# Kernel optimization log

Hardware: AMD Instinct MI355X
Metric: run time of the kernel (lower is better)

The kernel has to match this reference:

```python
import jax, jax.numpy as jnp
import numpy as np

B, N, LQ, DK, DV, DD = 2, 16, 512, 64, 64, 128
TEMPERATURE = 8.0  # sqrt(DK)
NEG_INF = -1e9


def setup_inputs() -> dict:
    key = jax.random.key(0)
    ks = jax.random.split(key, 9)
    h2 = 2 * DD  # dc hidden width = d0 + d1
    return {
        "q": jax.random.normal(ks[0], (B, N, LQ, DK), jnp.float32),
        "k": jax.random.normal(ks[1], (B, N, LQ, DK), jnp.float32),
        "v": jax.random.normal(ks[2], (B, N, LQ, DV), jnp.float32),
        "d0": jax.random.normal(ks[3], (B, LQ, DD), jnp.float32),
        "d1": jax.random.normal(ks[4], (B, LQ, DD), jnp.float32),
        "W1": jax.random.normal(ks[5], (h2, h2), jnp.float32) / np.sqrt(h2),
        "b1": jnp.zeros((h2,), jnp.float32),
        "W2": jax.random.normal(ks[6], (h2, 2), jnp.float32) / np.sqrt(h2),
        "b2": jnp.zeros((2,), jnp.float32),
    }


def reference(q, k, v, d0, d1, W1, b1, W2, b2):
    b, n, lq, dk = q.shape
    dd = d0.shape[-1]
    # pairwise features: f[b,i,j] = concat(d0[b,i], d1[b,j])  -> [b,lq,lq,2dd]
    f = jnp.concatenate(
        [
            jnp.broadcast_to(d0[:, :, None, :], (b, lq, lq, dd)),
            jnp.broadcast_to(d1[:, None, :, :], (b, lq, lq, dd)),
        ],
        axis=-1,
    )
    h = jax.nn.relu(jnp.einsum("bijf,fg->bijg", f, W1) + b1)
    logits = jnp.einsum("bijg,gc->bijc", h, W2) + b2  # [b,lq,lq,2]
    # eval-mode gumbel_softmax(hard=True, tau=1, training=False): argmax of logits
    decisions = (jnp.argmax(logits, axis=-1) == 1)[:, None, :, :]  # [b,1,lq,lq]
    attn = jnp.einsum("bnid,bnjd->bnij", q / TEMPERATURE, k)
    attn = jnp.where(decisions, attn, NEG_INF)
    attn = jax.nn.softmax(attn, axis=-1)  # dropout is identity in eval mode
    output = jnp.einsum("bnij,bnjd->bnid", attn, v)
    return output, attn, decisions
```

## Files before the change

kernel.cpp:

```cpp
#include <hip/hip_runtime.h>

#define BB 2
#define NN 16
#define LQ 512
#define DKk 64
#define DVv 64
#define DDd 128
#define H2 256
#define NEG_INF -1e9f

__global__ __launch_bounds__(256) void mlp_stage1(
    const float* __restrict__ d0, const float* __restrict__ d1,
    const float* __restrict__ W1, const float* __restrict__ b1,
    double* __restrict__ U64, double* __restrict__ W64,
    float* __restrict__ U32, float* __restrict__ W32)
{
    __shared__ float drow[2][DDd];
    int gid = blockIdx.x;
    int half = gid >> 9;
    int r0 = (gid & 511) * 2;
    const float* din = half ? d1 : d0;
    int w1off = half ? DDd : 0;
    double* o64 = half ? W64 : U64;
    float* o32 = half ? W32 : U32;
    int t = threadIdx.x;
    drow[t >> 7][t & 127] = din[(size_t)(r0 + (t >> 7)) * DDd + (t & 127)];
    __syncthreads();
    int g = t;
    double acc[2] = {};
#pragma unroll 2
    for (int f = 0; f < DDd; f += 4) {
        double w0 = (double)W1[(w1off + f + 0) * H2 + g];
        double w1 = (double)W1[(w1off + f + 1) * H2 + g];
        double w2 = (double)W1[(w1off + f + 2) * H2 + g];
        double w3 = (double)W1[(w1off + f + 3) * H2 + g];
#pragma unroll
        for (int r = 0; r < 2; ++r) {
            float4 dr = *(const float4*)&drow[r][f];
            acc[r] = fma((double)dr.x, w0, acc[r]);
            acc[r] = fma((double)dr.y, w1, acc[r]);
            acc[r] = fma((double)dr.z, w2, acc[r]);
            acc[r] = fma((double)dr.w, w3, acc[r]);
        }
    }
    double bb = half ? 0.0 : (double)b1[g];
#pragma unroll
    for (int r = 0; r < 2; ++r) {
        double a = acc[r] + bb;
        o64[(size_t)(r0 + r) * H2 + g] = a;
        o32[(size_t)(r0 + r) * H2 + g] = (float)a;
    }
}

__global__ __launch_bounds__(256, 2) void dec_full(
    const float* __restrict__ U32, const float* __restrict__ W32,
    const double* __restrict__ U64, const double* __restrict__ W64,
    const float* __restrict__ W2, const float* __restrict__ b2,
    float* __restrict__ dec_out)
{
    __shared__ __align__(16) float Ut[H2][36];
    __shared__ __align__(16) float Wt[H2][36];
    __shared__ float gvs[H2];
    __shared__ int lbuf[1024];
    __shared__ int lcnt;
    int bid = blockIdx.x;
    int b  = bid >> 8;
    int i0 = ((bid >> 4) & 15) * 32;
    int j0 = (bid & 15) * 32;
    int t = threadIdx.x;
    gvs[t] = W2[t * 2 + 1] - W2[t * 2];
    if (t == 0) lcnt = 0;
    float bias = b2[1] - b2[0];
    {
        int r = t >> 3, gq = t & 7;
        const float* su = U32 + ((size_t)(b * LQ) + i0 + r) * H2;
        const float* sw = W32 + ((size_t)(b * LQ) + j0 + r) * H2;
#pragma unroll
        for (int s = 0; s < 8; ++s) {
            int g = gq * 4 + s * 32;
            float4 u4 = *(const float4*)(su + g);
            Ut[g + 0][r] = u4.x; Ut[g + 1][r] = u4.y;
            Ut[g + 2][r] = u4.z; Ut[g + 3][r] = u4.w;
            float4 w4 = *(const float4*)(sw + g);
            Wt[g + 0][r] = w4.x; Wt[g + 1][r] = w4.y;
            Wt[g + 2][r] = w4.z; Wt[g + 3][r] = w4.w;
        }
    }
    __syncthreads();
    int pi = t >> 4, pj = t & 15;
    float a00 = 0.f, a01 = 0.f, a10 = 0.f, a11 = 0.f;
#pragma unroll 8
    for (int g = 0; g < H2; ++g) {
        float2 u2 = *(const float2*)&Ut[g][pi * 2];
        float2 w2 = *(const float2*)&Wt[g][pj * 2];
        float gv = gvs[g];
        a00 = fmaf(fmaxf(u2.x + w2.x, 0.f), gv, a00);
        a01 = fmaf(fmaxf(u2.x + w2.y, 0.f), gv, a01);
        a10 = fmaf(fmaxf(u2.y + w2.x, 0.f), gv, a10);
        a11 = fmaf(fmaxf(u2.y + w2.y, 0.f), gv, a11);
    }
    int row0 = b * LQ + i0 + pi * 2;
    float g00 = a00 + bias, g01 = a01 + bias;
    float g10 = a10 + bias, g11 = a11 + bias;
    int jb = j0 + pj * 2;
    *(float2*)&dec_out[(size_t)row0 * LQ + jb] =
        make_float2(g00 > 0.f ? 1.f : 0.f, g01 > 0.f ? 1.f : 0.f);
    *(float2*)&dec_out[(size_t)(row0 + 1) * LQ + jb] =
        make_float2(g10 > 0.f ? 1.f : 0.f, g11 > 0.f ? 1.f : 0.f);
    if (fabsf(g00) < 2e-2f) { int lx = atomicAdd(&lcnt, 1); lbuf[lx] = (row0 << 9) | jb; }
    if (fabsf(g01) < 2e-2f) { int lx = atomicAdd(&lcnt, 1); lbuf[lx] = (row0 << 9) | (jb + 1); }
    if (fabsf(g10) < 2e-2f) { int lx = atomicAdd(&lcnt, 1); lbuf[lx] = ((row0 + 1) << 9) | jb; }
    if (fabsf(g11) < 2e-2f) { int lx = atomicAdd(&lcnt, 1); lbuf[lx] = ((row0 + 1) << 9) | (jb + 1); }
    __syncthreads();
    int nloc = lcnt;
    int wv = t >> 6, ln = t & 63;
    for (int x = wv; x < nloc; x += 4) {
        int pij = lbuf[x];
        int j = pij & (LQ - 1);
        int prow = pij >> 9;
        int pb = prow >> 9;
        const double* u = U64 + (size_t)prow * H2;
        const double* w = W64 + ((size_t)(pb * LQ) + j) * H2;
        double acc = 0.0;
        for (int g = ln; g < H2; g += 64) {
            double tv = u[g] + w[g];
            tv = tv > 0.0 ? tv : 0.0;
            acc = fma(tv, (double)W2[g * 2 + 1] - (double)W2[g * 2 + 0], acc);
        }
#pragma unroll
        for (int off = 32; off; off >>= 1) acc += __shfl_xor(acc, off, 64);
        if (ln == 0) {
            acc += (double)b2[1] - (double)b2[0];
            dec_out[(size_t)prow * LQ + j] = acc > 0.0 ? 1.f : 0.f;
        }
    }
}

__global__ __launch_bounds__(256) void fused_attn(
    const float* __restrict__ q, const float* __restrict__ k,
    const float* __restrict__ v, const float* __restrict__ dec,
    float* __restrict__ attn, float* __restrict__ out)
{
    __shared__ __align__(16) float smem[10752];
    float* qT = smem;
    float* kT = smem + 2304;
    float* Ps = smem;
    float* Vs = smem + 2112;
    int bid = blockIdx.x;
    int bn = bid >> 4;
    int i0 = (bid & 15) * 32;
    int b = bn >> 4;
    int t = threadIdx.x;

    {
        int qi = t >> 3;
        const float* src = q + ((size_t)bn * LQ + i0 + qi) * DKk;
#pragma unroll
        for (int it = 0; it < 2; ++it) {
            int kkq = (t & 7) + it * 8;
            float4 t4 = *(const float4*)(src + kkq * 4);
            qT[(kkq * 4 + 0) * 36 + qi] = t4.x;
            qT[(kkq * 4 + 1) * 36 + qi] = t4.y;
            qT[(kkq * 4 + 2) * 36 + qi] = t4.z;
            qT[(kkq * 4 + 3) * 36 + qi] = t4.w;
        }
    }
    int tiq = t >> 5;
    int tjq = t & 31;
    float s[4][4][4];

#pragma unroll
    for (int c = 0; c < 4; ++c) {
        __syncthreads();
        {
            int kj = t >> 2;
#pragma unroll
            for (int it = 0; it < 8; ++it) {
                int jj = kj + (it & 1) * 64;
                int kkq = (t & 3) + (it >> 1) * 4;
                float4 t4 = *(const float4*)(k + ((size_t)bn * LQ + c * 128 + jj) * DKk + kkq * 4);
                kT[(kkq * 4 + 0) * 132 + jj] = t4.x;
                kT[(kkq * 4 + 1) * 132 + jj] = t4.y;
                kT[(kkq * 4 + 2) * 132 + jj] = t4.z;
                kT[(kkq * 4 + 3) * 132 + jj] = t4.w;
            }
        }
        __syncthreads();
        float acc[4][4] = {};
#pragma unroll 8
        for (int kk = 0; kk < 64; ++kk) {
            float4 a  = *(const float4*)&qT[kk * 36 + tiq * 4];
            float4 bb = *(const float4*)&kT[kk * 132 + tjq * 4];
            acc[0][0] = fmaf(a.x, bb.x, acc[0][0]); acc[0][1] = fmaf(a.x, bb.y, acc[0][1]);
            acc[0][2] = fmaf(a.x, bb.z, acc[0][2]); acc[0][3] = fmaf(a.x, bb.w, acc[0][3]);
            acc[1][0] = fmaf(a.y, bb.x, acc[1][0]); acc[1][1] = fmaf(a.y, bb.y, acc[1][1]);
            acc[1][2] = fmaf(a.y, bb.z, acc[1][2]); acc[1][3] = fmaf(a.y, bb.w, acc[1][3]);
            acc[2][0] = fmaf(a.z, bb.x, acc[2][0]); acc[2][1] = fmaf(a.z, bb.y, acc[2][1]);
            acc[2][2] = fmaf(a.z, bb.z, acc[2][2]); acc[2][3] = fmaf(a.z, bb.w, acc[2][3]);
            acc[3][0] = fmaf(a.w, bb.x, acc[3][0]); acc[3][1] = fmaf(a.w, bb.y, acc[3][1]);
            acc[3][2] = fmaf(a.w, bb.z, acc[3][2]); acc[3][3] = fmaf(a.w, bb.w, acc[3][3]);
        }
#pragma unroll
        for (int r = 0; r < 4; ++r) {
            float4 m4 = *(const float4*)&dec[((size_t)(b * LQ) + i0 + tiq * 4 + r) * LQ + c * 128 + tjq * 4];
            s[c][r][0] = m4.x != 0.f ? acc[r][0] * 0.125f : NEG_INF;
            s[c][r][1] = m4.y != 0.f ? acc[r][1] * 0.125f : NEG_INF;
            s[c][r][2] = m4.z != 0.f ? acc[r][2] * 0.125f : NEG_INF;
            s[c][r][3] = m4.w != 0.f ? acc[r][3] * 0.125f : NEG_INF;
        }
    }
#pragma unroll
    for (int r = 0; r < 4; ++r) {
        float m = NEG_INF;
#pragma unroll
        for (int c = 0; c < 4; ++c)
#pragma unroll
            for (int cc = 0; cc < 4; ++cc) m = fmaxf(m, s[c][r][cc]);
#pragma unroll
        for (int off = 1; off < 32; off <<= 1) m = fmaxf(m, __shfl_xor(m, off, 32));
        float sum = 0.f;
#pragma unroll
        for (int c = 0; c < 4; ++c)
#pragma unroll
            for (int cc = 0; cc < 4; ++cc) {
                float e = __expf(s[c][r][cc] - m);
                s[c][r][cc] = e; sum += e;
            }
#pragma unroll
        for (int off = 1; off < 32; off <<= 1) sum += __shfl_xor(sum, off, 32);
        float inv = 1.f / sum;
#pragma unroll
        for (int c = 0; c < 4; ++c)
#pragma unroll
            for (int cc = 0; cc < 4; ++cc) s[c][r][cc] *= inv;
    }
#pragma unroll
    for (int c = 0; c < 4; ++c)
#pragma unroll
        for (int r = 0; r < 4; ++r) {
            float4 wv = make_float4(s[c][r][0], s[c][r][1], s[c][r][2], s[c][r][3]);
            *(float4*)&attn[((size_t)bn * LQ + i0 + tiq * 4 + r) * LQ + c * 128 + tjq * 4] = wv;
        }
    int tio = t >> 4;
    int tdo = t & 15;
    float o[2][4] = {};
#pragma unroll
    for (int c8 = 0; c8 < 8; ++c8) {
        __syncthreads();
        if ((tjq >> 4) == (c8 & 1)) {
            int jl4 = tjq & 15;
            int c = c8 >> 1;
#pragma unroll
            for (int r = 0; r < 4; ++r)
#pragma unroll
                for (int cc = 0; cc < 4; ++cc)
                    Ps[(tiq * 4 + r) * 65 + jl4 * 4 + cc] = s[c][r][cc];
        }
        {
            int vj = t >> 2;
#pragma unroll
            for (int it = 0; it < 4; ++it) {
                int dq = (t & 3) + it * 4;
                *(float4*)&Vs[vj * 68 + dq * 4] =
                    *(const float4*)(v + ((size_t)bn * LQ + c8 * 64 + vj) * DVv + dq * 4);
            }
        }
        __syncthreads();
#pragma unroll 8
        for (int jj = 0; jj < 64; ++jj) {
            float p0 = Ps[(tio * 2 + 0) * 65 + jj];
            float p1 = Ps[(tio * 2 + 1) * 65 + jj];
            float4 v4 = *(const float4*)&Vs[jj * 68 + tdo * 4];
            o[0][0] = fmaf(p0, v4.x, o[0][0]); o[0][1] = fmaf(p0, v4.y, o[0][1]);
            o[0][2] = fmaf(p0, v4.z, o[0][2]); o[0][3] = fmaf(p0, v4.w, o[0][3]);
            o[1][0] = fmaf(p1, v4.x, o[1][0]); o[1][1] = fmaf(p1, v4.y, o[1][1]);
            o[1][2] = fmaf(p1, v4.z, o[1][2]); o[1][3] = fmaf(p1, v4.w, o[1][3]);
        }
    }
#pragma unroll
    for (int rr = 0; rr < 2; ++rr)
        *(float4*)&out[((size_t)bn * LQ + i0 + tio * 2 + rr) * DVv + tdo * 4] =
            make_float4(o[rr][0], o[rr][1], o[rr][2], o[rr][3]);
}

extern "C" void kernel_launch(void* const* d_in, const int* in_sizes, int n_in,
                              void* d_out, int out_size, void* d_ws, size_t ws_size,
                              hipStream_t stream)
{
    const float* q  = (const float*)d_in[0];
    const float* k  = (const float*)d_in[1];
    const float* v  = (const float*)d_in[2];
    const float* d0 = (const float*)d_in[3];
    const float* d1 = (const float*)d_in[4];
    const float* W1 = (const float*)d_in[5];
    const float* b1 = (const float*)d_in[6];
    const float* W2 = (const float*)d_in[7];
    const float* b2 = (const float*)d_in[8];

    float* out  = (float*)d_out;
    float* attn = out + (size_t)BB * NN * LQ * DVv;
    float* dec  = attn + (size_t)BB * NN * LQ * LQ;

    char* scratch = (char*)attn;
    double* U64 = (double*)(scratch);
    double* W64 = (double*)(scratch + (2u << 20));
    float*  U32 = (float*) (scratch + (4u << 20));
    float*  W32 = (float*) (scratch + (5u << 20));

    mlp_stage1<<<1024, 256, 0, stream>>>(d0, d1, W1, b1, U64, W64, U32, W32);
    dec_full<<<512, 256, 0, stream>>>(U32, W32, U64, W64, W2, b2, dec);
    fused_attn<<<512, 256, 0, stream>>>(q, k, v, dec, attn, out);
}
```

Before: 166.2 us.

## Use transposed swizzled P tile and split-K 4x4 register tiling for PV

Stores the softmax probabilities transposed in shared memory with an XOR swizzle, so each thread reads four query rows with a single float4 load. Each thread now computes a 4x4 output tile over half of the key dimension. The two halves are combined through shared memory at the end. This raises FMA-per-LDS-load reuse and removes the padded scalar P reads, at the cost of an extra reduction step, a barrier, and more accumulator registers.

Result: faster. 160.8 us (-3.3%).

```diff
diff --git a/kernel.cpp b/kernel.cpp
--- a/kernel.cpp
+++ b/kernel.cpp
@@ -144,7 +144,7 @@
     __shared__ __align__(16) float smem[10752];
     float* qT = smem;
     float* kT = smem + 2304;
-    float* Ps = smem;
+    float* Pt = smem;
     float* Vs = smem + 2112;
     int bid = blockIdx.x;
     int bn = bid >> 4;
@@ -241,9 +241,11 @@
             float4 wv = make_float4(s[c][r][0], s[c][r][1], s[c][r][2], s[c][r][3]);
             *(float4*)&attn[((size_t)bn * LQ + i0 + tiq * 4 + r) * LQ + c * 128 + tjq * 4] = wv;
         }
-    int tio = t >> 4;
-    int tdo = t & 15;
-    float o[2][4] = {};
+
+    int jh = t >> 7;
+    int ih = (t >> 4) & 7;
+    int dh = t & 15;
+    float o[4][4] = {};
 #pragma unroll
     for (int c8 = 0; c8 < 8; ++c8) {
         __syncthreads();
@@ -251,10 +253,11 @@
             int jl4 = tjq & 15;
             int c = c8 >> 1;
 #pragma unroll
-            for (int r = 0; r < 4; ++r)
-#pragma unroll
-                for (int cc = 0; cc < 4; ++cc)
-                    Ps[(tiq * 4 + r) * 65 + jl4 * 4 + cc] = s[c][r][cc];
+            for (int cc = 0; cc < 4; ++cc) {
+                int row = jl4 * 4 + cc;
+                *(float4*)&Pt[row * 32 + ((tiq ^ (row & 7)) << 2)] =
+                    make_float4(s[c][0][cc], s[c][1][cc], s[c][2][cc], s[c][3][cc]);
+            }
         }
         {
             int vj = t >> 2;
@@ -267,20 +270,40 @@
         }
         __syncthreads();
 #pragma unroll 8
-        for (int jj = 0; jj < 64; ++jj) {
-            float p0 = Ps[(tio * 2 + 0) * 65 + jj];
-            float p1 = Ps[(tio * 2 + 1) * 65 + jj];
-            float4 v4 = *(const float4*)&Vs[jj * 68 + tdo * 4];
-            o[0][0] = fmaf(p0, v4.x, o[0][0]); o[0][1] = fmaf(p0, v4.y, o[0][1]);
-            o[0][2] = fmaf(p0, v4.z, o[0][2]); o[0][3] = fmaf(p0, v4.w, o[0][3]);
-            o[1][0] = fmaf(p1, v4.x, o[1][0]); o[1][1] = fmaf(p1, v4.y, o[1][1]);
-            o[1][2] = fmaf(p1, v4.z, o[1][2]); o[1][3] = fmaf(p1, v4.w, o[1][3]);
-        }
-    }
-#pragma unroll
-    for (int rr = 0; rr < 2; ++rr)
-        *(float4*)&out[((size_t)bn * LQ + i0 + tio * 2 + rr) * DVv + tdo * 4] =
-            make_float4(o[rr][0], o[rr][1], o[rr][2], o[rr][3]);
+        for (int jx = 0; jx < 32; ++jx) {
+            int jj = jh * 32 + jx;
+            float4 p4 = *(const float4*)&Pt[jj * 32 + ((ih ^ (jj & 7)) << 2)];
+            float4 v4 = *(const float4*)&Vs[jj * 68 + dh * 4];
+            o[0][0] = fmaf(p4.x, v4.x, o[0][0]); o[0][1] = fmaf(p4.x, v4.y, o[0][1]);
+            o[0][2] = fmaf(p4.x, v4.z, o[0][2]); o[0][3] = fmaf(p4.x, v4.w, o[0][3]);
+            o[1][0] = fmaf(p4.y, v4.x, o[1][0]); o[1][1] = fmaf(p4.y, v4.y, o[1][1]);
+            o[1][2] = fmaf(p4.y, v4.z, o[1][2]); o[1][3] = fmaf(p4.y, v4.w, o[1][3]);
+            o[2][0] = fmaf(p4.z, v4.x, o[2][0]); o[2][1] = fmaf(p4.z, v4.y, o[2][1]);
+            o[2][2] = fmaf(p4.z, v4.z, o[2][2]); o[2][3] = fmaf(p4.z, v4.w, o[2][3]);
+            o[3][0] = fmaf(p4.w, v4.x, o[3][0]); o[3][1] = fmaf(p4.w, v4.y, o[3][1]);
+            o[3][2] = fmaf(p4.w, v4.z, o[3][2]); o[3][3] = fmaf(p4.w, v4.w, o[3][3]);
+        }
+    }
+    __syncthreads();
+    float* red = smem;
+    if (jh == 1) {
+        int kidx = (ih * 16 + dh) * 20;
+#pragma unroll
+        for (int rr = 0; rr < 4; ++rr)
+            *(float4*)&red[kidx + rr * 4] =
+                make_float4(o[rr][0], o[rr][1], o[rr][2], o[rr][3]);
+    }
+    __syncthreads();
+    if (jh == 0) {
+        int kidx = (ih * 16 + dh) * 20;
+#pragma unroll
+        for (int rr = 0; rr < 4; ++rr) {
+            float4 p = *(const float4*)&red[kidx + rr * 4];
+            *(float4*)&out[((size_t)bn * LQ + i0 + ih * 4 + rr) * DVv + dh * 4] =
+                make_float4(o[rr][0] + p.x, o[rr][1] + p.y,
+                            o[rr][2] + p.z, o[rr][3] + p.w);
+        }
+    }
 }
 
 extern "C" void kernel_launch(void* const* d_in, const int* in_sizes, int n_in,
```
